# Performance work log

Measured on AMD Instinct MI355X. Metric: run time of the kernel, lower is better.

Reference implementation:

```python
import jax, jax.numpy as jnp
import numpy as np
from jax import lax

N = 50000      # num_nodes
D = 128        # hidden_dim
P = 6          # num_path
L1 = 6         # path_length1
L2 = 4         # path_length2


def setup_inputs() -> dict:
    key = jax.random.key(0)
    k1, k2, k3, k4, k5, k6 = jax.random.split(key, 6)
    feats = jax.random.normal(k1, (N, D), dtype=jnp.float32)
    init_feats = jax.random.normal(k2, (N, D), dtype=jnp.float32)
    paths = jax.random.randint(k3, (P, N, L1), 0, N, dtype=jnp.int64)
    # xavier_normal with gain=1.414 for (1, L, D): std = gain*sqrt(2/(L+D)) on fan dims of last two axes
    std1 = 1.414 * np.sqrt(2.0 / (L1 + D))
    std2 = 1.414 * np.sqrt(2.0 / (L2 + D))
    std_fc = 1.414 * np.sqrt(2.0 / (D + D))
    path_weight1 = jax.random.normal(k4, (1, L1, D), dtype=jnp.float32) * std1
    path_weight2 = jax.random.normal(k5, (1, L2, D), dtype=jnp.float32) * std2
    fc_weight = jax.random.normal(k6, (D, D), dtype=jnp.float32) * std_fc  # Linear weight (out, in)
    return {
        "feats": feats,
        "paths": paths,
        "init_feats": init_feats,
        "flag": 1,
        "path_weight1": path_weight1,
        "path_weight2": path_weight2,
        "fc_weight": fc_weight,
    }


def reference(feats, paths, init_feats, flag, path_weight1, path_weight2, fc_weight):
    # flag is a Python int constant selecting which path-weight bank to use
    w = path_weight1[0] if flag == 1 else path_weight2[0]  # (L, D)
    num_path = paths.shape[0]

    def body(acc, p):
        # p: (N, L) node indices; gather (N, L, D), weighted-sum over path dim
        pf = feats[p]                       # (N, L, D)
        acc = acc + jnp.einsum("nld,ld->nd", pf, w)
        return acc, None

    acc, _ = lax.scan(body, jnp.zeros((feats.shape[0], feats.shape[1]), feats.dtype), paths)
    results = acc / num_path
    out = jax.nn.relu(results @ fc_weight.T)  # Linear(bias=False): x @ W^T
    return out
```

## Files before the change

### kernel.cpp

```cpp
#include <hip/hip_runtime.h>
#include <stdint.h>

#define NN 50000
#define DD 128
#define PP 6
#define LL 6
#define NPG 4
#define WPAD 136

typedef float f4 __attribute__((ext_vector_type(4)));
typedef short bf16x8 __attribute__((ext_vector_type(8)));

__device__ __forceinline__ uint16_t f2bf(float f) {
  uint32_t u = __float_as_uint(f);
  u = (u + 0x7fffu + ((u >> 16) & 1u)) >> 16;
  return (uint16_t)u;
}
__device__ __forceinline__ float bf_lo(uint32_t u) { return __uint_as_float(u << 16); }
__device__ __forceinline__ float bf_hi(uint32_t u) { return __uint_as_float(u & 0xffff0000u); }

__global__ __launch_bounds__(256) void k_cvt(const float* __restrict__ in,
                                             uint16_t* __restrict__ out, int n4) {
  int i = blockIdx.x * 256 + threadIdx.x;
  if (i >= n4) return;
  f4 v = ((const f4*)in)[i];
  ushort4 o;
  o.x = f2bf(v.x); o.y = f2bf(v.y); o.z = f2bf(v.z); o.w = f2bf(v.w);
  ((ushort4*)out)[i] = o;
}

__global__ __launch_bounds__(256) void k_gather(
    const uint16_t* __restrict__ fb,
    const int* __restrict__ paths,
    const float* __restrict__ w,
    float* __restrict__ acc) {
  const int lane = threadIdx.x & 31;
  const int grp  = threadIdx.x >> 5;
  const int d0   = lane * 4;
  const int nbase = blockIdx.x * (8 * NPG) + grp * NPG;

  f4 wl[LL];
  #pragma unroll
  for (int l = 0; l < LL; ++l)
    wl[l] = *(const f4*)(w + l * DD + d0);

  #pragma unroll
  for (int ni = 0; ni < NPG; ++ni) {
    const int n = nbase + ni;
    if (n >= NN) return;
    f4 a = {0.f, 0.f, 0.f, 0.f};
    #pragma unroll
    for (int p = 0; p < PP; ++p) {
      #pragma unroll
      for (int l = 0; l < LL; ++l) {
        const int idx = paths[(p * NN + n) * LL + l];
        const uint2 v = *(const uint2*)(fb + idx * DD + d0);
        a.x = fmaf(wl[l].x, bf_lo(v.x), a.x);
        a.y = fmaf(wl[l].y, bf_hi(v.x), a.y);
        a.z = fmaf(wl[l].z, bf_lo(v.y), a.z);
        a.w = fmaf(wl[l].w, bf_hi(v.y), a.w);
      }
    }
    const float s = 1.f / 6.f;
    a.x *= s; a.y *= s; a.z *= s; a.w *= s;
    *(f4*)(acc + (size_t)n * DD + d0) = a;
  }
}

__global__ __launch_bounds__(256) void k_fc(
    const float* __restrict__ acc,
    const float* __restrict__ fcw,
    float* __restrict__ out) {
  __shared__ uint16_t sA[64 * WPAD];
  __shared__ uint16_t sW[128 * WPAD];
  const int t = threadIdx.x;
  const int nb = blockIdx.x * 64;

  #pragma unroll
  for (int it = 0; it < 8; ++it) {
    const int chunk = it * 256 + t;
    const int row = chunk >> 5, c4 = chunk & 31;
    f4 v = {0.f, 0.f, 0.f, 0.f};
    if (nb + row < NN) v = *(const f4*)(acc + (size_t)(nb + row) * DD + c4 * 4);
    ushort4 o;
    o.x = f2bf(v.x); o.y = f2bf(v.y); o.z = f2bf(v.z); o.w = f2bf(v.w);
    *(ushort4*)(sA + row * WPAD + c4 * 4) = o;
  }
  #pragma unroll
  for (int it = 0; it < 16; ++it) {
    const int chunk = it * 256 + t;
    const int row = chunk >> 5, c4 = chunk & 31;
    f4 v = *(const f4*)(fcw + row * DD + c4 * 4);
    ushort4 o;
    o.x = f2bf(v.x); o.y = f2bf(v.y); o.z = f2bf(v.z); o.w = f2bf(v.w);
    *(ushort4*)(sW + row * WPAD + c4 * 4) = o;
  }
  __syncthreads();

  const int w  = t >> 6;
  const int l  = t & 63;
  const int lr = l & 15;
  const int hk = (l >> 4) * 8;

  bf16x8 afrag[4];
  #pragma unroll
  for (int k0 = 0; k0 < 4; ++k0)
    afrag[k0] = *(bf16x8*)(sA + (w * 16 + lr) * WPAD + k0 * 32 + hk);

  #pragma unroll
  for (int o = 0; o < 8; ++o) {
    f4 dacc = {0.f, 0.f, 0.f, 0.f};
    #pragma unroll
    for (int k0 = 0; k0 < 4; ++k0) {
      bf16x8 bfrag = *(bf16x8*)(sW + (o * 16 + lr) * WPAD + k0 * 32 + hk);
      dacc = __builtin_amdgcn_mfma_f32_16x16x32_bf16(afrag[k0], bfrag, dacc, 0, 0, 0);
    }
    const int col = o * 16 + lr;
    #pragma unroll
    for (int r = 0; r < 4; ++r) {
      const int n = nb + w * 16 + (l >> 4) * 4 + r;
      if (n < NN) out[(size_t)n * DD + col] = fmaxf(dacc[r], 0.f);
    }
  }
}

extern "C" void kernel_launch(void* const* d_in, const int* in_sizes, int n_in,
                              void* d_out, int out_size, void* d_ws, size_t ws_size,
                              hipStream_t stream) {
  const float* feats = (const float*)d_in[0];
  const int*   paths = (const int*)d_in[1];
  const float* pw1   = (const float*)d_in[4];
  const float* fcw   = (const float*)d_in[6];
  float* out = (float*)d_out;

  uint16_t* fb  = (uint16_t*)d_ws;
  float*    acc = (float*)((char*)d_ws + (size_t)NN * DD * 2);

  const int n4 = NN * DD / 4;
  k_cvt<<<(n4 + 255) / 256, 256, 0, stream>>>(feats, fb, n4);
  k_gather<<<(NN + 8 * NPG - 1) / (8 * NPG), 256, 0, stream>>>(fb, paths, pw1, acc);
  k_fc<<<(NN + 63) / 64, 256, 0, stream>>>(acc, fcw, out);
}
```

Before: 84.66 us.

## Stage path indices in LDS, batch gathers, and store bf16 intermediate

The gather kernel now loads each block's 64 nodes' path indices into shared memory with coalesced reads, then issues all 36 row gathers per node before the FMAs to raise memory-level parallelism. The 1/6 scale is folded into the weights. The intermediate accumulator is written as bf16 instead of fp32, which halves that write and the fc kernel's read and removes its conversion step. The costs are extra register pressure from 36 in-flight loads and one more bf16 rounding of the accumulator, a rounding the fc kernel already performed before its MFMA.

```diff
diff --git a/kernel.cpp b/kernel.cpp
--- a/kernel.cpp
+++ b/kernel.cpp
@@ -5,7 +5,7 @@
 #define DD 128
 #define PP 6
 #define LL 6
-#define NPG 4
+#define GN 64
 #define WPAD 136
 
 typedef float f4 __attribute__((ext_vector_type(4)));
@@ -33,42 +33,69 @@
     const uint16_t* __restrict__ fb,
     const int* __restrict__ paths,
     const float* __restrict__ w,
-    float* __restrict__ acc) {
-  const int lane = threadIdx.x & 31;
-  const int grp  = threadIdx.x >> 5;
+    uint16_t* __restrict__ accb) {
+  __shared__ int sidx[PP * GN * LL];
+  const int t = threadIdx.x;
+  const int nb = blockIdx.x * GN;
+
+  #pragma unroll
+  for (int s = 0; s < 9; ++s) {
+    const int i = s * 256 + t;
+    const int p = i / (GN * LL);
+    const int rem = i - p * (GN * LL);
+    const long g = (long)nb * LL + rem;
+    int val = 0;
+    if (g < (long)NN * LL) val = paths[(size_t)p * NN * LL + g];
+    sidx[i] = val;
+  }
+
+  const int lane = t & 31;
+  const int grp  = t >> 5;
   const int d0   = lane * 4;
-  const int nbase = blockIdx.x * (8 * NPG) + grp * NPG;
 
+  const float sc = 1.f / 6.f;
   f4 wl[LL];
   #pragma unroll
-  for (int l = 0; l < LL; ++l)
-    wl[l] = *(const f4*)(w + l * DD + d0);
+  for (int l = 0; l < LL; ++l) {
+    f4 v = *(const f4*)(w + l * DD + d0);
+    wl[l].x = v.x * sc; wl[l].y = v.y * sc; wl[l].z = v.z * sc; wl[l].w = v.w * sc;
+  }
 
-  #pragma unroll
-  for (int ni = 0; ni < NPG; ++ni) {
-    const int n = nbase + ni;
-    if (n >= NN) return;
+  __syncthreads();
+
+  #pragma unroll 1
+  for (int s = 0; s < 8; ++s) {
+    const int ni = grp * 8 + s;
+    const int n = nb + ni;
+    uint2 v[PP * LL];
+    #pragma unroll
+    for (int p = 0; p < PP; ++p)
+      #pragma unroll
+      for (int l = 0; l < LL; ++l) {
+        const int idx = sidx[(p * GN + ni) * LL + l];
+        v[p * LL + l] = *(const uint2*)(fb + (size_t)idx * DD + d0);
+      }
     f4 a = {0.f, 0.f, 0.f, 0.f};
     #pragma unroll
-    for (int p = 0; p < PP; ++p) {
+    for (int p = 0; p < PP; ++p)
       #pragma unroll
       for (int l = 0; l < LL; ++l) {
-        const int idx = paths[(p * NN + n) * LL + l];
-        const uint2 v = *(const uint2*)(fb + idx * DD + d0);
-        a.x = fmaf(wl[l].x, bf_lo(v.x), a.x);
-        a.y = fmaf(wl[l].y, bf_hi(v.x), a.y);
-        a.z = fmaf(wl[l].z, bf_lo(v.y), a.z);
-        a.w = fmaf(wl[l].w, bf_hi(v.y), a.w);
+        const uint2 u = v[p * LL + l];
+        a.x = fmaf(wl[l].x, bf_lo(u.x), a.x);
+        a.y = fmaf(wl[l].y, bf_hi(u.x), a.y);
+        a.z = fmaf(wl[l].z, bf_lo(u.y), a.z);
+        a.w = fmaf(wl[l].w, bf_hi(u.y), a.w);
       }
+    if (n < NN) {
+      ushort4 o;
+      o.x = f2bf(a.x); o.y = f2bf(a.y); o.z = f2bf(a.z); o.w = f2bf(a.w);
+      *(ushort4*)(accb + (size_t)n * DD + d0) = o;
     }
-    const float s = 1.f / 6.f;
-    a.x *= s; a.y *= s; a.z *= s; a.w *= s;
-    *(f4*)(acc + (size_t)n * DD + d0) = a;
   }
 }
 
 __global__ __launch_bounds__(256) void k_fc(
-    const float* __restrict__ acc,
+    const uint16_t* __restrict__ accb,
     const float* __restrict__ fcw,
     float* __restrict__ out) {
   __shared__ uint16_t sA[64 * WPAD];
@@ -77,14 +104,12 @@
   const int nb = blockIdx.x * 64;
 
   #pragma unroll
-  for (int it = 0; it < 8; ++it) {
+  for (int it = 0; it < 4; ++it) {
     const int chunk = it * 256 + t;
-    const int row = chunk >> 5, c4 = chunk & 31;
-    f4 v = {0.f, 0.f, 0.f, 0.f};
-    if (nb + row < NN) v = *(const f4*)(acc + (size_t)(nb + row) * DD + c4 * 4);
-    ushort4 o;
-    o.x = f2bf(v.x); o.y = f2bf(v.y); o.z = f2bf(v.z); o.w = f2bf(v.w);
-    *(ushort4*)(sA + row * WPAD + c4 * 4) = o;
+    const int row = chunk >> 4, c8 = chunk & 15;
+    uint4 v = {0u, 0u, 0u, 0u};
+    if (nb + row < NN) v = *(const uint4*)(accb + (size_t)(nb + row) * DD + c8 * 8);
+    *(uint4*)(sA + row * WPAD + c8 * 8) = v;
   }
   #pragma unroll
   for (int it = 0; it < 16; ++it) {
@@ -133,11 +158,11 @@
   const float* fcw   = (const float*)d_in[6];
   float* out = (float*)d_out;
 
-  uint16_t* fb  = (uint16_t*)d_ws;
-  float*    acc = (float*)((char*)d_ws + (size_t)NN * DD * 2);
+  uint16_t* fb   = (uint16_t*)d_ws;
+  uint16_t* accb = (uint16_t*)((char*)d_ws + (size_t)NN * DD * 2);
 
   const int n4 = NN * DD / 4;
   k_cvt<<<(n4 + 255) / 256, 256, 0, stream>>>(feats, fb, n4);
-  k_gather<<<(NN + 8 * NPG - 1) / (8 * NPG), 256, 0, stream>>>(fb, paths, pw1, acc);
-  k_fc<<<(NN + 63) / 64, 256, 0, stream>>>(acc, fcw, out);
+  k_gather<<<(NN + GN - 1) / GN, 256, 0, stream>>>(fb, paths, pw1, accb);
+  k_fc<<<(NN + 63) / 64, 256, 0, stream>>>(accb, fcw, out);
 }
```

New measurement: 82.40 us. -2.7%, faster.
